# Performance work log

Hardware: AMD Instinct MI355X
Metric: run time of the kernel (lower is better)

Reference implementation:

```python
import jax, jax.numpy as jnp
import numpy as np

# POLLU: 25 reactions, 20 species. Each flux r_i = k_i * C[a_i] * C[b_i],
# where index 20 points at a constant-ones row (unimolecular reactions).
ONES_ROW = 20
IDX_A = np.array([0, 1, 4, 6, 6, 6, 8, 8, 10, 10, 12, 9, 13, 0, 2, 3, 3, 15, 15, 16, 18, 18, 0, 18, 19], dtype=np.int32)
IDX_B = np.array([ONES_ROW, 3, 1, ONES_ROW, ONES_ROW, 5, ONES_ROW, 5, 1, 0, ONES_ROW, 1, ONES_ROW, 5, ONES_ROW, ONES_ROW, ONES_ROW, ONES_ROW, ONES_ROW, 5, ONES_ROW, ONES_ROW, 3, 0, ONES_ROW], dtype=np.int32)

def _stoich():
    # species -> list of (coef, 1-based reaction id), transcribed from dy0..dy19
    ent = {
        0: [(-1,1),(-1,10),(-1,14),(-1,23),(-1,24),(1,2),(1,3),(1,9),(1,11),(1,12),(1,22),(1,25)],
        1: [(-1,2),(-1,3),(-1,9),(-1,12),(1,1),(1,21)],
        2: [(-1,15),(1,1),(1,17),(1,19),(1,22)],
        3: [(-1,2),(-1,16),(-1,17),(-1,23),(1,15)],
        4: [(-1,3),(2,4),(1,6),(1,7),(1,13),(1,20)],
        5: [(-1,6),(-1,8),(-1,14),(-1,20),(1,3),(2,18)],
        6: [(-1,4),(-1,5),(-1,6),(1,13)],
        7: [(1,4),(1,5),(1,6),(1,7)],
        8: [(-1,7),(-1,8)],
        9: [(-1,12),(1,7),(1,9)],
        10: [(-1,9),(-1,10),(1,8),(1,11)],
        11: [(1,9)],
        12: [(-1,11),(1,10)],
        13: [(-1,13),(1,12)],
        14: [(1,14)],
        15: [(-1,18),(-1,19),(1,16)],
        16: [(-1,20)],
        17: [(1,20)],
        18: [(-1,21),(-1,22),(-1,24),(1,23),(1,25)],
        19: [(-1,25),(1,24)],
    }
    S = np.zeros((20, 25), dtype=np.float32)
    for sp, lst in ent.items():
        for c, r in lst:
            S[sp, r - 1] += c
    return S

S = _stoich()  # [20 species, 25 reactions]
B = 2_000_000


def setup_inputs() -> dict:
    key = jax.random.key(0)
    k1, k2 = jax.random.split(key)
    conc_in = jax.random.uniform(k1, (20, B), dtype=jnp.float32)
    k = jax.random.uniform(k2, (25,), dtype=jnp.float32)
    t = jnp.zeros((1,), dtype=jnp.float32)
    return {"t": t, "conc_in": conc_in, "k": k}


def reference(t, conc_in, k):
    # conc_in: [20, B]. Append ones row so every flux is a product of two gathers.
    C = jnp.concatenate([conc_in, jnp.ones((1, conc_in.shape[1]), conc_in.dtype)], axis=0)  # [21, B]
    flux = k[:, None] * C[IDX_A] * C[IDX_B]  # [25, B]
    dy = jnp.einsum('sr,rb->bs', jnp.asarray(S, dtype=conc_in.dtype), flux)  # [B, 20]
    return dy
```

## Files before the change

### kernel.cpp

```cpp
#include <hip/hip_runtime.h>

#define B_TOTAL 2000000

__global__ __launch_bounds__(256) void pollu_kernel(
    const float* __restrict__ conc,
    const float* __restrict__ k,
    float* __restrict__ out)
{
    __shared__ float sk[25];
    if (threadIdx.x < 25) sk[threadIdx.x] = k[threadIdx.x];
    __syncthreads();

    const int b = blockIdx.x * blockDim.x + threadIdx.x;
    if (b >= B_TOTAL) return;

    const size_t B = (size_t)B_TOTAL;
    float c[20];
#pragma unroll
    for (int s = 0; s < 20; ++s) c[s] = conc[(size_t)s * B + (size_t)b];

    const float f1  = sk[0]  * c[0];
    const float f2  = sk[1]  * c[1]  * c[3];
    const float f3  = sk[2]  * c[4]  * c[1];
    const float f4  = sk[3]  * c[6];
    const float f5  = sk[4]  * c[6];
    const float f6  = sk[5]  * c[6]  * c[5];
    const float f7  = sk[6]  * c[8];
    const float f8  = sk[7]  * c[8]  * c[5];
    const float f9  = sk[8]  * c[10] * c[1];
    const float f10 = sk[9]  * c[10] * c[0];
    const float f11 = sk[10] * c[12];
    const float f12 = sk[11] * c[9]  * c[1];
    const float f13 = sk[12] * c[13];
    const float f14 = sk[13] * c[0]  * c[5];
    const float f15 = sk[14] * c[2];
    const float f16 = sk[15] * c[3];
    const float f17 = sk[16] * c[3];
    const float f18 = sk[17] * c[15];
    const float f19 = sk[18] * c[15];
    const float f20 = sk[19] * c[16] * c[5];
    const float f21 = sk[20] * c[18];
    const float f22 = sk[21] * c[18];
    const float f23 = sk[22] * c[0]  * c[3];
    const float f24 = sk[23] * c[18] * c[0];
    const float f25 = sk[24] * c[19];

    const float dy0  = -f1 - f10 - f14 - f23 - f24 + f2 + f3 + f9 + f11 + f12 + f22 + f25;
    const float dy1  = -f2 - f3 - f9 - f12 + f1 + f21;
    const float dy2  = -f15 + f1 + f17 + f19 + f22;
    const float dy3  = -f2 - f16 - f17 - f23 + f15;
    const float dy4  = -f3 + 2.0f * f4 + f6 + f7 + f13 + f20;
    const float dy5  = -f6 - f8 - f14 - f20 + f3 + 2.0f * f18;
    const float dy6  = -f4 - f5 - f6 + f13;
    const float dy7  =  f4 + f5 + f6 + f7;
    const float dy8  = -f7 - f8;
    const float dy9  = -f12 + f7 + f9;
    const float dy10 = -f9 - f10 + f8 + f11;
    const float dy11 =  f9;
    const float dy12 = -f11 + f10;
    const float dy13 = -f13 + f12;
    const float dy14 =  f14;
    const float dy15 = -f18 - f19 + f16;
    const float dy16 = -f20;
    const float dy17 =  f20;
    const float dy18 = -f21 - f22 - f24 + f23 + f25;
    const float dy19 = -f25 + f24;

    float4* o = (float4*)(out + (size_t)b * 20u);
    o[0] = make_float4(dy0,  dy1,  dy2,  dy3);
    o[1] = make_float4(dy4,  dy5,  dy6,  dy7);
    o[2] = make_float4(dy8,  dy9,  dy10, dy11);
    o[3] = make_float4(dy12, dy13, dy14, dy15);
    o[4] = make_float4(dy16, dy17, dy18, dy19);
}

extern "C" void kernel_launch(void* const* d_in, const int* in_sizes, int n_in,
                              void* d_out, int out_size, void* d_ws, size_t ws_size,
                              hipStream_t stream) {
    const float* conc = (const float*)d_in[1];
    const float* k    = (const float*)d_in[2];
    float* out        = (float*)d_out;

    const int block = 256;
    const int grid  = (B_TOTAL + block - 1) / block;
    pollu_kernel<<<grid, block, 0, stream>>>(conc, k, out);
}
```

Before: 287.5 us.

## Process four batch elements per thread with vectorized nontemporal loads

```diff
diff --git a/kernel.cpp b/kernel.cpp
--- a/kernel.cpp
+++ b/kernel.cpp
@@ -1,87 +1,106 @@
 #include <hip/hip_runtime.h>
 
 #define B_TOTAL 2000000
+#define NT (B_TOTAL / 4)
+
+typedef float floatx4 __attribute__((ext_vector_type(4)));
 
 __global__ __launch_bounds__(256) void pollu_kernel(
-    const float* __restrict__ conc,
+    const floatx4* __restrict__ conc4,
     const float* __restrict__ k,
-    float* __restrict__ out)
+    floatx4* __restrict__ out4)
 {
-    __shared__ float sk[25];
-    if (threadIdx.x < 25) sk[threadIdx.x] = k[threadIdx.x];
-    __syncthreads();
+    const int g = blockIdx.x * 256 + threadIdx.x;
+    if (g >= NT) return;
 
-    const int b = blockIdx.x * blockDim.x + threadIdx.x;
-    if (b >= B_TOTAL) return;
+    floatx4 c4[20];
+#pragma unroll
+    for (int s = 0; s < 20; ++s)
+        c4[s] = __builtin_nontemporal_load(&conc4[(size_t)s * NT + (size_t)g]);
 
-    const size_t B = (size_t)B_TOTAL;
-    float c[20];
+    const float k1  = k[0],  k2  = k[1],  k3  = k[2],  k4  = k[3],  k5  = k[4];
+    const float k6  = k[5],  k7  = k[6],  k8  = k[7],  k9  = k[8],  k10 = k[9];
+    const float k11 = k[10], k12 = k[11], k13 = k[12], k14 = k[13], k15 = k[14];
+    const float k16 = k[15], k17 = k[16], k18 = k[17], k19 = k[18], k20 = k[19];
+    const float k21 = k[20], k22 = k[21], k23 = k[22], k24 = k[23], k25 = k[24];
+
+    const float* cf = (const float*)c4;
+
 #pragma unroll
-    for (int s = 0; s < 20; ++s) c[s] = conc[(size_t)s * B + (size_t)b];
+    for (int j = 0; j < 4; ++j) {
+        float c[20];
+#pragma unroll
+        for (int s = 0; s < 20; ++s) c[s] = cf[4 * s + j];
 
-    const float f1  = sk[0]  * c[0];
-    const float f2  = sk[1]  * c[1]  * c[3];
-    const float f3  = sk[2]  * c[4]  * c[1];
-    const float f4  = sk[3]  * c[6];
-    const float f5  = sk[4]  * c[6];
-    const float f6  = sk[5]  * c[6]  * c[5];
-    const float f7  = sk[6]  * c[8];
-    const float f8  = sk[7]  * c[8]  * c[5];
-    const float f9  = sk[8]  * c[10] * c[1];
-    const float f10 = sk[9]  * c[10] * c[0];
-    const float f11 = sk[10] * c[12];
-    const float f12 = sk[11] * c[9]  * c[1];
-    const float f13 = sk[12] * c[13];
-    const float f14 = sk[13] * c[0]  * c[5];
-    const float f15 = sk[14] * c[2];
-    const float f16 = sk[15] * c[3];
-    const float f17 = sk[16] * c[3];
-    const float f18 = sk[17] * c[15];
-    const float f19 = sk[18] * c[15];
-    const float f20 = sk[19] * c[16] * c[5];
-    const float f21 = sk[20] * c[18];
-    const float f22 = sk[21] * c[18];
-    const float f23 = sk[22] * c[0]  * c[3];
-    const float f24 = sk[23] * c[18] * c[0];
-    const float f25 = sk[24] * c[19];
+        const float f1  = k1  * c[0];
+        const float f2  = k2  * c[1]  * c[3];
+        const float f3  = k3  * c[4]  * c[1];
+        const float f4  = k4  * c[6];
+        const float f5  = k5  * c[6];
+        const float f6  = k6  * c[6]  * c[5];
+        const float f7  = k7  * c[8];
+        const float f8  = k8  * c[8]  * c[5];
+        const float f9  = k9  * c[10] * c[1];
+        const float f10 = k10 * c[10] * c[0];
+        const float f11 = k11 * c[12];
+        const float f12 = k12 * c[9]  * c[1];
+        const float f13 = k13 * c[13];
+        const float f14 = k14 * c[0]  * c[5];
+        const float f15 = k15 * c[2];
+        const float f16 = k16 * c[3];
+        const float f17 = k17 * c[3];
+        const float f18 = k18 * c[15];
+        const float f19 = k19 * c[15];
+        const float f20 = k20 * c[16] * c[5];
+        const float f21 = k21 * c[18];
+        const float f22 = k22 * c[18];
+        const float f23 = k23 * c[0]  * c[3];
+        const float f24 = k24 * c[18] * c[0];
+        const float f25 = k25 * c[19];
 
-    const float dy0  = -f1 - f10 - f14 - f23 - f24 + f2 + f3 + f9 + f11 + f12 + f22 + f25;
-    const float dy1  = -f2 - f3 - f9 - f12 + f1 + f21;
-    const float dy2  = -f15 + f1 + f17 + f19 + f22;
-    const float dy3  = -f2 - f16 - f17 - f23 + f15;
-    const float dy4  = -f3 + 2.0f * f4 + f6 + f7 + f13 + f20;
-    const float dy5  = -f6 - f8 - f14 - f20 + f3 + 2.0f * f18;
-    const float dy6  = -f4 - f5 - f6 + f13;
-    const float dy7  =  f4 + f5 + f6 + f7;
-    const float dy8  = -f7 - f8;
-    const float dy9  = -f12 + f7 + f9;
-    const float dy10 = -f9 - f10 + f8 + f11;
-    const float dy11 =  f9;
-    const float dy12 = -f11 + f10;
-    const float dy13 = -f13 + f12;
-    const float dy14 =  f14;
-    const float dy15 = -f18 - f19 + f16;
-    const float dy16 = -f20;
-    const float dy17 =  f20;
-    const float dy18 = -f21 - f22 - f24 + f23 + f25;
-    const float dy19 = -f25 + f24;
+        const float dy0  = -f1 - f10 - f14 - f23 - f24 + f2 + f3 + f9 + f11 + f12 + f22 + f25;
+        const float dy1  = -f2 - f3 - f9 - f12 + f1 + f21;
+        const float dy2  = -f15 + f1 + f17 + f19 + f22;
+        const float dy3  = -f2 - f16 - f17 - f23 + f15;
+        const float dy4  = -f3 + 2.0f * f4 + f6 + f7 + f13 + f20;
+        const float dy5  = -f6 - f8 - f14 - f20 + f3 + 2.0f * f18;
+        const float dy6  = -f4 - f5 - f6 + f13;
+        const float dy7  =  f4 + f5 + f6 + f7;
+        const float dy8  = -f7 - f8;
+        const float dy9  = -f12 + f7 + f9;
+        const float dy10 = -f9 - f10 + f8 + f11;
+        const float dy11 =  f9;
+        const float dy12 = -f11 + f10;
+        const float dy13 = -f13 + f12;
+        const float dy14 =  f14;
+        const float dy15 = -f18 - f19 + f16;
+        const float dy16 = -f20;
+        const float dy17 =  f20;
+        const float dy18 = -f21 - f22 - f24 + f23 + f25;
+        const float dy19 = -f25 + f24;
 
-    float4* o = (float4*)(out + (size_t)b * 20u);
-    o[0] = make_float4(dy0,  dy1,  dy2,  dy3);
-    o[1] = make_float4(dy4,  dy5,  dy6,  dy7);
-    o[2] = make_float4(dy8,  dy9,  dy10, dy11);
-    o[3] = make_float4(dy12, dy13, dy14, dy15);
-    o[4] = make_float4(dy16, dy17, dy18, dy19);
+        floatx4* o = out4 + (size_t)g * 20u + (size_t)(5 * j);
+        floatx4 o0 = {dy0,  dy1,  dy2,  dy3};
+        floatx4 o1 = {dy4,  dy5,  dy6,  dy7};
+        floatx4 o2 = {dy8,  dy9,  dy10, dy11};
+        floatx4 o3 = {dy12, dy13, dy14, dy15};
+        floatx4 o4 = {dy16, dy17, dy18, dy19};
+        o[0] = o0;
+        o[1] = o1;
+        o[2] = o2;
+        o[3] = o3;
+        o[4] = o4;
+    }
 }
 
 extern "C" void kernel_launch(void* const* d_in, const int* in_sizes, int n_in,
                               void* d_out, int out_size, void* d_ws, size_t ws_size,
                               hipStream_t stream) {
-    const float* conc = (const float*)d_in[1];
-    const float* k    = (const float*)d_in[2];
-    float* out        = (float*)d_out;
+    const floatx4* conc4 = (const floatx4*)d_in[1];
+    const float* k       = (const float*)d_in[2];
+    floatx4* out4        = (floatx4*)d_out;
 
     const int block = 256;
-    const int grid  = (B_TOTAL + block - 1) / block;
-    pollu_kernel<<<grid, block, 0, stream>>>(conc, k, out);
+    const int grid  = (NT + block - 1) / block;
+    pollu_kernel<<<grid, block, 0, stream>>>(conc4, k, out4);
 }
```

New measurement: 303.3 us. 5.5% more time.
